# Performance work log

Hardware: AMD Instinct MI355X
Metric: run time of the kernel (lower is better)

Reference implementation:

```python
import jax, jax.numpy as jnp
import numpy as np

W_BITS = 8       # default precision = max(precisions)
MIN_PREC = 4     # min(precisions)
GROUP_SIZE = 128


def make_new_byte_indices(total_bytes: int) -> np.ndarray:
    # Replicates make_new_byte_indices_torch. Note: in the torch code,
    # argsort(argsort(new_idx)) == new_idx (it is a permutation), so the
    # "unpermute" is a gather with new_idx itself.
    bytes_per_thread = 4
    threads_per_warp = 32
    bytes_per_warp = threads_per_warp * bytes_per_thread  # 128
    full = total_bytes // bytes_per_warp * bytes_per_warp
    rem = total_bytes - full
    parts = []
    if full > 0:
        bi = np.arange(full)
        warp_offsets = (bi // bytes_per_warp) * bytes_per_warp
        thread_indices = bi % threads_per_warp
        byte_off = ((bi % bytes_per_warp) // threads_per_warp) ^ 3
        parts.append(warp_offsets + thread_indices * bytes_per_thread + byte_off)
    if rem > 0:
        ri = np.arange(rem)
        adj = rem // bytes_per_thread
        if adj > 0:
            warp_offsets = (ri // bytes_per_warp) * bytes_per_warp
            thread_indices = ri % adj
            byte_off = (ri // adj) ^ 3
            parts.append(warp_offsets + thread_indices * 4 + byte_off + full)
        else:
            parts.append(np.arange(full, full + rem))
    return np.concatenate(parts).astype(np.int64)


def dequant(qweight, scale, zero, w_bits=W_BITS):
    _, N, in_chunks = qweight.shape
    total_bytes = in_chunks * 4
    in_features = in_chunks * 32
    q = qweight[:w_bits]
    # little-endian byte view of int32 (matches torch .view(torch.uint8))
    b = jnp.stack([(q >> (8 * k)) & 0xFF for k in range(4)], axis=-1)
    b = b.reshape(w_bits, N, total_bytes)  # int32 values in [0,255]
    idx = jnp.asarray(make_new_byte_indices(total_bytes))
    b = b[:, :, idx]
    # unpack bits, MSB first within each byte
    bits = jnp.stack([(b >> i) & 1 for i in reversed(range(8))], axis=-1)
    bits = bits.reshape(w_bits, N, in_features)  # [w_bits, N, in_features]
    plane_w = jnp.asarray([1 << (w_bits - 1 - k) for k in range(w_bits)], dtype=jnp.int32)
    qw = jnp.einsum('b,bni->ni', plane_w, bits)  # int32 in [0, 2^w_bits-1]
    weight_f = qw.astype(jnp.float32)
    bit_err = w_bits - MIN_PREC
    zero = zero * (2.0 ** bit_err)
    scale_pc = jnp.repeat(scale, GROUP_SIZE, axis=1)[:, :in_features]
    zero_pc = jnp.repeat(zero, GROUP_SIZE, axis=1)[:, :in_features]
    return scale_pc * (weight_f - zero_pc)  # [N, in_features]


def setup_inputs() -> dict:
    key = jax.random.key(0)
    kx, kq, ks, kz, kb = jax.random.split(key, 5)
    B, S, IN, OUT, G = 4, 2048, 4096, 4096, GROUP_SIZE
    x = jax.random.normal(kx, (B, S, IN), dtype=jnp.float32)
    qweight = jax.random.randint(kq, (8, OUT, IN // 32), 0, 2147483647, dtype=jnp.int32)
    scale = jax.random.uniform(ks, (OUT, IN // G), dtype=jnp.float32) * 0.01 + 1e-4
    zero = jax.random.uniform(kz, (OUT, IN // G), dtype=jnp.float32) * 8.0
    bias = jax.random.normal(kb, (OUT,), dtype=jnp.float32)
    return {"x": x, "qweight": qweight, "scale": scale, "zero": zero, "bias": bias}


def reference(x, qweight, scale, zero, bias):
    weight = dequant(qweight, scale, zero, W_BITS)  # [out, in]
    return jnp.matmul(x, weight.T) + bias
```

## Files before the change

### kernel.cpp

```cpp
#include <hip/hip_runtime.h>
#include <hip/hip_bf16.h>
#include <stdint.h>

typedef __attribute__((ext_vector_type(8))) short short8;
typedef __attribute__((ext_vector_type(4))) float f32x4;

#define M_DIM 8192
#define N_DIM 4096
#define K_DIM 4096
#define BM 256
#define BN 256
#define BK 64

static __device__ __forceinline__ unsigned short f32_to_bf16(float f) {
  union { float f; unsigned int u; } v; v.f = f;
  unsigned int u = v.u;
  u += 0x7fffu + ((u >> 16) & 1u);
  return (unsigned short)(u >> 16);
}

__global__ void cast_x_kernel(const float* __restrict__ x,
                              unsigned short* __restrict__ xb) {
  size_t i = ((size_t)blockIdx.x * blockDim.x + threadIdx.x) * 8;
  if (i >= (size_t)M_DIM * K_DIM) return;
  float4 v0 = *reinterpret_cast<const float4*>(x + i);
  float4 v1 = *reinterpret_cast<const float4*>(x + i + 4);
  short8 o;
  o[0] = (short)f32_to_bf16(v0.x);
  o[1] = (short)f32_to_bf16(v0.y);
  o[2] = (short)f32_to_bf16(v0.z);
  o[3] = (short)f32_to_bf16(v0.w);
  o[4] = (short)f32_to_bf16(v1.x);
  o[5] = (short)f32_to_bf16(v1.y);
  o[6] = (short)f32_to_bf16(v1.z);
  o[7] = (short)f32_to_bf16(v1.w);
  *reinterpret_cast<short8*>(xb + i) = o;
}

__global__ void dequant_kernel(const int* __restrict__ qw,
                               const float* __restrict__ scale,
                               const float* __restrict__ zero,
                               unsigned short* __restrict__ W) {
  int idx = blockIdx.x * blockDim.x + threadIdx.x;
  if (idx >= N_DIM * 128) return;
  int n = idx >> 7;
  int c = idx & 127;
  unsigned int w[8];
#pragma unroll
  for (int k = 0; k < 8; ++k)
    w[k] = (unsigned int)qw[(size_t)k * (N_DIM * 128) + idx];
  int wp = c >> 5, t = c & 31;
#pragma unroll
  for (int s = 0; s < 4; ++s) {
    int r = s ^ 3;
    unsigned int by[8];
#pragma unroll
    for (int k = 0; k < 8; ++k) by[k] = (w[k] >> (8 * r)) & 0xffu;
    int ibase = wp * 1024 + s * 256 + t * 8;
    int g = ibase >> 7;
    float sc = scale[n * 32 + g];
    float zp = zero[n * 32 + g] * 16.0f;
    short8 o;
#pragma unroll
    for (int u = 0; u < 8; ++u) {
      unsigned int q = 0;
#pragma unroll
      for (int k = 0; k < 8; ++k)
        q |= ((by[k] >> (7 - u)) & 1u) << (7 - k);
      o[u] = (short)f32_to_bf16(sc * ((float)q - zp));
    }
    *reinterpret_cast<short8*>(&W[(size_t)n * K_DIM + ibase]) = o;
  }
}


#define VMCNT2 asm volatile("s_waitcnt vmcnt(2)" ::: "memory")
#define VMCNT0 asm volatile("s_waitcnt vmcnt(0)" ::: "memory")
#define LGKM8  asm volatile("s_waitcnt lgkmcnt(8)" ::: "memory")
#define NOOP ((void)0)

#define STG(G, GROWB, KT, LDSC) do {                                           \
  const unsigned short* sb_ = (G) + ((size_t)(GROWB) * K_DIM + (KT) * 64);     \
  __builtin_amdgcn_global_load_lds(                                            \
      (const __attribute__((address_space(1))) void*)(sb_ + s_off0),           \
      (__attribute__((address_space(3))) void*)(smem + (LDSC) + wslot),        \
      16, 0, 0);                                                               \
  __builtin_amdgcn_global_load_lds(                                            \
      (const __attribute__((address_space(1))) void*)(sb_ + s_off1),           \
      (__attribute__((address_space(3))) void*)(smem + (LDSC) + 8192 + wslot), \
      16, 0, 0);                                                               \
} while (0)
#define STG_A(BUF, H, KT) STG(Ag, m0 + (H)*128, (KT), ((BUF)*2 + (H)) * 16384)
#define STG_B(BUF, H, KT) STG(Bg, n0 + (H)*128, (KT), 65536 + ((BUF)*2 + (H)) * 16384)

#define LOAD_A(BUF, QM) do {                                                   \
  _Pragma("unroll") for (int mf_ = 0; mf_ < 4; ++mf_) {                        \
    a_[mf_][0] = *(const short8*)(smem + a_off0 +                              \
                                  (((BUF)*2 + (QM)) * 16384 + mf_ * 2048));    \
    a_[mf_][1] = *(const short8*)(smem + a_off1 +                              \
                                  (((BUF)*2 + (QM)) * 16384 + mf_ * 2048));    \
  } } while (0)

#define LOAD_B(BUF, QN) do {                                                   \
  _Pragma("unroll") for (int nf_ = 0; nf_ < 2; ++nf_) {                        \
    b_[nf_][0] = *(const short8*)(smem + b_off0 +                              \
                                  (((BUF)*2 + (QN)) * 16384 + nf_ * 2048));    \
    b_[nf_][1] = *(const short8*)(smem + b_off1 +                              \
                                  (((BUF)*2 + (QN)) * 16384 + nf_ * 2048));    \
  } } while (0)

#define PHASE(LOADS, QM, QN, STAGE, TAIL) do {                                 \
  LOADS;                                                                       \
  STAGE;                                                                       \
  __builtin_amdgcn_s_barrier();                                                \
  asm volatile("s_waitcnt lgkmcnt(0)" ::: "memory");                           \
  __builtin_amdgcn_sched_barrier(0);                                           \
  __builtin_amdgcn_s_setprio(1);                                               \
  _Pragma("unroll") for (int mf_ = 0; mf_ < 4; ++mf_)                          \
    _Pragma("unroll") for (int nf_ = 0; nf_ < 2; ++nf_)                        \
      _Pragma("unroll") for (int kk_ = 0; kk_ < 2; ++kk_)                      \
        acc[QM][QN][mf_][nf_] = __builtin_amdgcn_mfma_f32_16x16x32_bf16(       \
            a_[mf_][kk_], b_[nf_][kk_], acc[QM][QN][mf_][nf_], 0, 0, 0);       \
  __builtin_amdgcn_s_setprio(0);                                               \
  TAIL;                                                                        \
  __builtin_amdgcn_s_barrier();                                                \
} while (0)

__global__ __launch_bounds__(512, 2) void gemm_kernel(
    const unsigned short* __restrict__ Ag,
    const unsigned short* __restrict__ Bg,
    const float* __restrict__ bias,
    float* __restrict__ C) {
  __shared__ __align__(16) char smem[131072];

  int bid = blockIdx.x;
  int cpx = gridDim.x >> 3;
  int swz = (bid & 7) * cpx + (bid >> 3);
  int tm = swz >> 4;
  int tn = swz & 15;
  int m0 = tm * BM, n0 = tn * BN;

  int tid = threadIdx.x;
  int lane = tid & 63;
  int wid = tid >> 6;
  int wr = wid >> 2, wc = wid & 3;

  const int xorv = (lane & 7) << 4;
  const int hi4 = (lane >> 4) << 4;
  const int wrbase = wr * 64 + (lane & 15);
  const int wcbase = wc * 32 + (lane & 15);
  const int a_off0 = (wrbase << 7) + (hi4 ^ xorv);
  const int a_off1 = (wrbase << 7) + ((64 | hi4) ^ xorv);
  const int b_off0 = 65536 + (wcbase << 7) + (hi4 ^ xorv);
  const int b_off1 = 65536 + (wcbase << 7) + ((64 | hi4) ^ xorv);
  const int wslot = (tid >> 6) << 10;
  const int s_lr0 = tid >> 3, s_lr1 = 64 + (tid >> 3);
  const int s_off0 = s_lr0 * K_DIM + (((tid & 7) ^ (s_lr0 & 7)) << 3);
  const int s_off1 = s_lr1 * K_DIM + (((tid & 7) ^ (s_lr1 & 7)) << 3);

  short8 a_[4][2], b_[2][2];
  f32x4 acc[2][2][4][2];
#pragma unroll
  for (int i = 0; i < 2; ++i)
#pragma unroll
    for (int j = 0; j < 2; ++j)
#pragma unroll
      for (int mf = 0; mf < 4; ++mf)
#pragma unroll
        for (int nf = 0; nf < 2; ++nf) acc[i][j][mf][nf] = (f32x4){0.f, 0.f, 0.f, 0.f};

  STG_A(0, 0, 0); STG_A(0, 1, 0); STG_B(0, 0, 0); STG_B(0, 1, 0);
  STG_A(1, 0, 1);
  VMCNT2;
  __builtin_amdgcn_s_barrier();

  for (int t = 0; t < 31; ++t) {
    const int kt1 = 2 * t + 1;
    PHASE(LOAD_A(0,0); LOAD_B(0,0), 0, 0, STG_B(1,0,kt1); LGKM8, NOOP);
    PHASE(LOAD_B(0,1),              0, 1, STG_A(1,1,kt1),        NOOP);
    PHASE(LOAD_A(0,1),              1, 1, STG_B(1,1,kt1),        NOOP);
    PHASE(LOAD_B(0,0),              1, 0, STG_A(0,0,kt1+1),      VMCNT2);
    PHASE(LOAD_A(1,0); LOAD_B(1,0), 0, 0, STG_B(0,1,kt1+1); LGKM8, NOOP);
    PHASE(LOAD_B(1,1),              0, 1, STG_A(0,1,kt1+1),      NOOP);
    PHASE(LOAD_A(1,1),              1, 1, STG_B(0,0,kt1+1),      NOOP);
    PHASE(LOAD_B(1,0),              1, 0, STG_A(1,0,kt1+2),      VMCNT2);
  }
  PHASE(LOAD_A(0,0); LOAD_B(0,0), 0, 0, STG_B(1,0,63); LGKM8, NOOP);
  PHASE(LOAD_B(0,1),              0, 1, STG_A(1,1,63),        NOOP);
  PHASE(LOAD_A(0,1),              1, 1, STG_B(1,1,63),        NOOP);
  PHASE(LOAD_B(0,0),              1, 0, NOOP,                 VMCNT0);
  PHASE(LOAD_A(1,0); LOAD_B(1,0), 0, 0, NOOP, NOOP);
  PHASE(LOAD_B(1,1),              0, 1, NOOP, NOOP);
  PHASE(LOAD_A(1,1),              1, 1, NOOP, NOOP);
  PHASE(LOAD_B(1,0),              1, 0, NOOP, NOOP);

#pragma unroll
  for (int qn = 0; qn < 2; ++qn)
#pragma unroll
    for (int nf = 0; nf < 2; ++nf) {
      int gcol = n0 + qn * 128 + wc * 32 + nf * 16 + (lane & 15);
      float bv = bias[gcol];
#pragma unroll
      for (int qm = 0; qm < 2; ++qm)
#pragma unroll
        for (int mf = 0; mf < 4; ++mf) {
          int grow = m0 + qm * 128 + wr * 64 + mf * 16 + ((lane >> 4) << 2);
          f32x4 v = acc[qm][qn][mf][nf];
#pragma unroll
          for (int j = 0; j < 4; ++j)
            C[(size_t)(grow + j) * N_DIM + gcol] = v[j] + bv;
        }
    }
}

extern "C" void kernel_launch(void* const* d_in, const int* in_sizes, int n_in,
                              void* d_out, int out_size, void* d_ws, size_t ws_size,
                              hipStream_t stream) {
  const float* x       = (const float*)d_in[0];
  const int*   qweight = (const int*)d_in[1];
  const float* scale   = (const float*)d_in[2];
  const float* zero    = (const float*)d_in[3];
  const float* bias    = (const float*)d_in[4];
  float* out = (float*)d_out;

  unsigned short* Xb = (unsigned short*)d_ws;
  unsigned short* Wb = Xb + (size_t)M_DIM * K_DIM;

  cast_x_kernel<<<(M_DIM * K_DIM / 8) / 256, 256, 0, stream>>>(x, Xb);
  dequant_kernel<<<(N_DIM * 128) / 256, 256, 0, stream>>>(qweight, scale, zero, Wb);
  gemm_kernel<<<(M_DIM / BM) * (N_DIM / BN), 512, 0, stream>>>(Xb, Wb, bias, out);
}
```

Measured before the change: 273.6 us.

## Overlap LDS fragment reads with MFMA and drop per-phase trailing barrier

Restructures the GEMM main loop so the LDS reads for the next sub-tile are issued between the two k-halves of the MFMA chain instead of before them, with one barrier per region instead of two. Global-to-LDS staging is moved inside the priority-raised region and gated by a vmcnt wait at the start of every region. The stage order is reshuffled to match the new read schedule. This is meant to hide LDS latency behind matrix math and cut barrier overhead, at the risk of races on the LDS buffers or wait counts that are wrong for the new order.

```diff
diff --git a/kernel.cpp b/kernel.cpp
--- a/kernel.cpp
+++ b/kernel.cpp
@@ -76,7 +76,6 @@
 
 #define VMCNT2 asm volatile("s_waitcnt vmcnt(2)" ::: "memory")
 #define VMCNT0 asm volatile("s_waitcnt vmcnt(0)" ::: "memory")
-#define LGKM8  asm volatile("s_waitcnt lgkmcnt(8)" ::: "memory")
 #define NOOP ((void)0)
 
 #define STG(G, GROWB, KT, LDSC) do {                                           \
@@ -93,37 +92,36 @@
 #define STG_A(BUF, H, KT) STG(Ag, m0 + (H)*128, (KT), ((BUF)*2 + (H)) * 16384)
 #define STG_B(BUF, H, KT) STG(Bg, n0 + (H)*128, (KT), 65536 + ((BUF)*2 + (H)) * 16384)
 
-#define LOAD_A(BUF, QM) do {                                                   \
-  _Pragma("unroll") for (int mf_ = 0; mf_ < 4; ++mf_) {                        \
-    a_[mf_][0] = *(const short8*)(smem + a_off0 +                              \
-                                  (((BUF)*2 + (QM)) * 16384 + mf_ * 2048));    \
-    a_[mf_][1] = *(const short8*)(smem + a_off1 +                              \
-                                  (((BUF)*2 + (QM)) * 16384 + mf_ * 2048));    \
-  } } while (0)
-
-#define LOAD_B(BUF, QN) do {                                                   \
-  _Pragma("unroll") for (int nf_ = 0; nf_ < 2; ++nf_) {                        \
-    b_[nf_][0] = *(const short8*)(smem + b_off0 +                              \
-                                  (((BUF)*2 + (QN)) * 16384 + nf_ * 2048));    \
-    b_[nf_][1] = *(const short8*)(smem + b_off1 +                              \
-                                  (((BUF)*2 + (QN)) * 16384 + nf_ * 2048));    \
-  } } while (0)
-
-#define PHASE(LOADS, QM, QN, STAGE, TAIL) do {                                 \
-  LOADS;                                                                       \
-  STAGE;                                                                       \
+#define LA(BUF, QM, KK) do {                                                   \
+  _Pragma("unroll") for (int mf_ = 0; mf_ < 4; ++mf_)                          \
+    a_[mf_][KK] = *(const short8*)(smem + ((KK) ? a_off1 : a_off0) +           \
+        (((BUF)*2 + (QM)) * 16384 + mf_ * 2048));                              \
+} while (0)
+#define LB(BUF, QN, KK) do {                                                   \
+  _Pragma("unroll") for (int nf_ = 0; nf_ < 2; ++nf_)                          \
+    b_[nf_][KK] = *(const short8*)(smem + ((KK) ? b_off1 : b_off0) +           \
+        (((BUF)*2 + (QN)) * 16384 + nf_ * 2048));                              \
+} while (0)
+
+#define MFMA_KK(QM, QN, KK)                                                    \
+  _Pragma("unroll") for (int mf_ = 0; mf_ < 4; ++mf_)                          \
+    _Pragma("unroll") for (int nf_ = 0; nf_ < 2; ++nf_)                        \
+      acc[QM][QN][mf_][nf_] = __builtin_amdgcn_mfma_f32_16x16x32_bf16(         \
+          a_[mf_][KK], b_[nf_][KK], acc[QM][QN][mf_][nf_], 0, 0, 0)
+
+#define REGION(QM, QN, RD0, RD1, STAGE, WAITV) do {                            \
   __builtin_amdgcn_s_barrier();                                                \
+  WAITV;                                                                       \
   asm volatile("s_waitcnt lgkmcnt(0)" ::: "memory");                           \
   __builtin_amdgcn_sched_barrier(0);                                           \
   __builtin_amdgcn_s_setprio(1);                                               \
-  _Pragma("unroll") for (int mf_ = 0; mf_ < 4; ++mf_)                          \
-    _Pragma("unroll") for (int nf_ = 0; nf_ < 2; ++nf_)                        \
-      _Pragma("unroll") for (int kk_ = 0; kk_ < 2; ++kk_)                      \
-        acc[QM][QN][mf_][nf_] = __builtin_amdgcn_mfma_f32_16x16x32_bf16(       \
-            a_[mf_][kk_], b_[nf_][kk_], acc[QM][QN][mf_][nf_], 0, 0, 0);       \
+  STAGE;                                                                       \
+  MFMA_KK(QM, QN, 0);                                                          \
+  RD0;                                                                         \
+  __builtin_amdgcn_sched_barrier(0);                                           \
+  MFMA_KK(QM, QN, 1);                                                          \
+  RD1;                                                                         \
   __builtin_amdgcn_s_setprio(0);                                               \
-  TAIL;                                                                        \
-  __builtin_amdgcn_s_barrier();                                                \
 } while (0)
 
 __global__ __launch_bounds__(512, 2) void gemm_kernel(
@@ -169,30 +167,31 @@
 #pragma unroll
         for (int nf = 0; nf < 2; ++nf) acc[i][j][mf][nf] = (f32x4){0.f, 0.f, 0.f, 0.f};
 
-  STG_A(0, 0, 0); STG_A(0, 1, 0); STG_B(0, 0, 0); STG_B(0, 1, 0);
+  STG_B(0, 0, 0); STG_A(0, 0, 0); STG_B(0, 1, 0); STG_A(0, 1, 0);
   STG_A(1, 0, 1);
   VMCNT2;
   __builtin_amdgcn_s_barrier();
+  LA(0, 0, 0); LB(0, 0, 0); LA(0, 0, 1); LB(0, 0, 1);
 
   for (int t = 0; t < 31; ++t) {
     const int kt1 = 2 * t + 1;
-    PHASE(LOAD_A(0,0); LOAD_B(0,0), 0, 0, STG_B(1,0,kt1); LGKM8, NOOP);
-    PHASE(LOAD_B(0,1),              0, 1, STG_A(1,1,kt1),        NOOP);
-    PHASE(LOAD_A(0,1),              1, 1, STG_B(1,1,kt1),        NOOP);
-    PHASE(LOAD_B(0,0),              1, 0, STG_A(0,0,kt1+1),      VMCNT2);
-    PHASE(LOAD_A(1,0); LOAD_B(1,0), 0, 0, STG_B(0,1,kt1+1); LGKM8, NOOP);
-    PHASE(LOAD_B(1,1),              0, 1, STG_A(0,1,kt1+1),      NOOP);
-    PHASE(LOAD_A(1,1),              1, 1, STG_B(0,0,kt1+1),      NOOP);
-    PHASE(LOAD_B(1,0),              1, 0, STG_A(1,0,kt1+2),      VMCNT2);
+    REGION(0, 0, LB(0,1,0),            LB(0,1,1),            STG_B(1,0,kt1),   VMCNT2);
+    REGION(0, 1, LA(0,1,0),            LA(0,1,1),            STG_B(1,1,kt1),   VMCNT2);
+    REGION(1, 1, LB(0,0,0),            LB(0,0,1),            STG_A(1,1,kt1),   VMCNT2);
+    REGION(1, 0, LA(1,0,0); LB(1,0,0), LA(1,0,1); LB(1,0,1), STG_B(0,0,kt1+1), VMCNT2);
+    REGION(0, 0, LB(1,1,0),            LB(1,1,1),            STG_A(0,0,kt1+1), VMCNT2);
+    REGION(0, 1, LA(1,1,0),            LA(1,1,1),            STG_B(0,1,kt1+1), VMCNT2);
+    REGION(1, 1, LB(1,0,0),            LB(1,0,1),            STG_A(0,1,kt1+1), VMCNT2);
+    REGION(1, 0, LA(0,0,0); LB(0,0,0), LA(0,0,1); LB(0,0,1), STG_A(1,0,kt1+2), VMCNT2);
   }
-  PHASE(LOAD_A(0,0); LOAD_B(0,0), 0, 0, STG_B(1,0,63); LGKM8, NOOP);
-  PHASE(LOAD_B(0,1),              0, 1, STG_A(1,1,63),        NOOP);
-  PHASE(LOAD_A(0,1),              1, 1, STG_B(1,1,63),        NOOP);
-  PHASE(LOAD_B(0,0),              1, 0, NOOP,                 VMCNT0);
-  PHASE(LOAD_A(1,0); LOAD_B(1,0), 0, 0, NOOP, NOOP);
-  PHASE(LOAD_B(1,1),              0, 1, NOOP, NOOP);
-  PHASE(LOAD_A(1,1),              1, 1, NOOP, NOOP);
-  PHASE(LOAD_B(1,0),              1, 0, NOOP, NOOP);
+  REGION(0, 0, LB(0,1,0),            LB(0,1,1),            STG_B(1,0,63), VMCNT2);
+  REGION(0, 1, LA(0,1,0),            LA(0,1,1),            STG_B(1,1,63), VMCNT2);
+  REGION(1, 1, LB(0,0,0),            LB(0,0,1),            STG_A(1,1,63), VMCNT2);
+  REGION(1, 0, LA(1,0,0); LB(1,0,0), LA(1,0,1); LB(1,0,1), NOOP,          VMCNT2);
+  REGION(0, 0, LB(1,1,0),            LB(1,1,1),            NOOP,          VMCNT0);
+  REGION(0, 1, LA(1,1,0),            LA(1,1,1),            NOOP,          NOOP);
+  REGION(1, 1, LB(1,0,0),            LB(1,0,1),            NOOP,          NOOP);
+  REGION(1, 0, NOOP,                 NOOP,                 NOOP,          NOOP);
 
 #pragma unroll
   for (int qn = 0; qn < 2; ++qn)
```

New measurement: 263.0 us. 1.04x faster.
